# Kernel optimization log

Measured on AMD Instinct MI355X. Metric: run time of the kernel, lower is better.

## Reference

```python
import jax, jax.numpy as jnp
import numpy as np

H_WINDOW = 8
X_WINDOW = 8
H_LAG = 0
X_LAG = 0
CHANNELS = 1
B, T = 8192, 2048


def setup_inputs() -> dict:
    key = jax.random.key(0)
    k1, k2, k3 = jax.random.split(key, 3)
    h = jax.random.normal(k1, (B, T, 1), dtype=jnp.float32)
    # torch init: normal(0, 0.05)
    h_weights = 0.05 * jax.random.normal(k2, (H_WINDOW, CHANNELS), dtype=jnp.float32)
    x_weights = 0.05 * jax.random.normal(k3, (X_WINDOW, CHANNELS), dtype=jnp.float32)
    biases = jnp.zeros((1, CHANNELS), dtype=jnp.float32)
    return {"h": h, "h_weights": h_weights, "x_weights": x_weights, "biases": biases}


def reference(h, h_weights, x_weights, biases):
    b, t, _ = h.shape
    start_ix = max(H_WINDOW + H_LAG - 1, X_WINDOW, X_LAG - 1)
    h_t = jnp.transpose(h, (1, 0, 2))              # [T, B, 1] time-major for per-step gather
    hw0 = h[:, :H_WINDOW].reshape(b, H_WINDOW)     # initial h window
    xw0 = jnp.zeros((b, X_WINDOW), dtype=h.dtype)  # initial x window (zeros, as in torch)

    def step(carry, i):
        hw_, xw_ = carry  # [B, H_WINDOW], [B, X_WINDOW]
        out = xw_ @ x_weights + hw_ @ h_weights + biases  # [B, CHANNELS]
        # window updates; at the final step the torch code skips the update but the
        # carry is discarded, so an index-clamped unconditional update is equivalent
        idx = jnp.minimum(i + 1 - H_LAG, t - 1)
        hw_n = jnp.concatenate([hw_, h_t[idx]], axis=1)[:, -H_WINDOW:]
        xw_n = jnp.concatenate([xw_, out], axis=1)[:, -X_WINDOW:]
        return (hw_n, xw_n), out

    _, outs = jax.lax.scan(step, (hw0, xw0), jnp.arange(start_ix, t))  # [T-start_ix, B, C]
    output = jnp.zeros((b, t, CHANNELS), dtype=h.dtype)
    output = output.at[:, start_ix:].set(jnp.transpose(outs, (1, 0, 2)))
    return output
```

## Files before the change

### kernel.cpp

```cpp
#include <hip/hip_runtime.h>


typedef float  f32x4  __attribute__((ext_vector_type(4)));
typedef short  bf16x8 __attribute__((ext_vector_type(8)));

#define TT 2048
#define BB 8192
#define LK 64
#define NTAPS 71

__device__ __forceinline__ unsigned short f2bfu(float x) {
    unsigned u = __float_as_uint(x);
    return (unsigned short)((u + 0x7FFFu + ((u >> 16) & 1u)) >> 16);
}
__device__ __forceinline__ float bf2f(short s) {
    return __uint_as_float(((unsigned)(unsigned short)s) << 16);
}

__device__ __forceinline__ void group8(const float hwt[8], const float xwt[8],
                                       float bs, const float win[8],
                                       const float nh[8], const float xq[8],
                                       float res[8])
{
#pragma unroll
    for (int u = 0; u < 8; ++u) {
        float acc = bs;
#pragma unroll
        for (int k = u; k < 8; ++k) acc = fmaf(win[k], hwt[k - u], acc);
#pragma unroll
        for (int k = 0; k < u; ++k) acc = fmaf(nh[k], hwt[8 - u + k], acc);
#pragma unroll
        for (int k = u; k < 8; ++k) acc = fmaf(xq[k], xwt[k - u], acc);
#pragma unroll
        for (int k = 0; k < u; ++k) acc = fmaf(res[k], xwt[8 - u + k], acc);
        res[u] = acc;
    }
}

__global__ void rr_setup(const float* __restrict__ hwt_g, const float* __restrict__ xwt_g,
                         const float* __restrict__ bias_g, float* __restrict__ ws)
{
    if (threadIdx.x != 0 || blockIdx.x != 0) return;
    float hwt[8], xwt[8];
#pragma unroll
    for (int j = 0; j < 8; ++j) { hwt[j] = hwt_g[j]; xwt[j] = xwt_g[j]; }
    float K[LK];
    K[0] = 1.f;
    float ksum = 1.f;
#pragma unroll
    for (int n = 1; n < LK; ++n) {
        float a = 0.f;
#pragma unroll
        for (int j = 0; j < 8; ++j) {
            const int idx = n - 8 + j;
            if (idx >= 0) a = fmaf(xwt[j], K[idx], a);
        }
        K[n] = a; ksum += a;
    }
#pragma unroll
    for (int d = 0; d < NTAPS; ++d) {
        float a = 0.f;
#pragma unroll
        for (int j = 0; j < 8; ++j) {
            const int n = d - 7 + j;
            if (n >= 0 && n < LK) a = fmaf(hwt[j], K[n], a);
        }
        ws[d] = a;
    }
    ws[NTAPS] = bias_g[0] * ksum;
}

__global__ __launch_bounds__(256) void rr_mfma(
    const float* __restrict__ h, const float* __restrict__ hwt_g,
    const float* __restrict__ xwt_g, const float* __restrict__ bias_g,
    const float* __restrict__ cws, float* __restrict__ out)
{
    __shared__ short hlds[16][584];
    __shared__ float cl[72];

    const int t   = threadIdx.x;
    const int bid = blockIdx.x;
    const int strip = bid & 3;
    const int r0    = (bid >> 2) << 4;

    const int ts     = (strip < 3) ? (5 + 31 * strip) : 98;
    const int ntiles = (strip < 3) ? 31 : 30;
    const int gcol0  = 16 * ts - 80;
    const int nf4    = (strip < 3) ? 144 : 140;

    if (t < 72) cl[t] = cws[t];

    {
        const int row = t >> 4, l16 = t & 15;
        const float* hrow = h + (size_t)(r0 + row) * TT + gcol0;
#pragma unroll
        for (int k = 0; k < 9; ++k) {
            const int c = l16 + 16 * k;
            if (c < nf4) {
                float4 v = reinterpret_cast<const float4*>(hrow)[c];
                uint2 pk;
                pk.x = (unsigned)f2bfu(v.x) | ((unsigned)f2bfu(v.y) << 16);
                pk.y = (unsigned)f2bfu(v.z) | ((unsigned)f2bfu(v.w) << 16);
                *reinterpret_cast<uint2*>(&hlds[row][4 * c]) = pk;
            }
        }
    }
    __syncthreads();

    const int lane = t & 63;
    const int v    = lane & 15;
    const int gq   = lane >> 4;
    const int w    = t >> 6;

    const float biasK = cl[71];

    bf16x8 bfr[3];
#pragma unroll
    for (int kb = 0; kb < 3; ++kb) {
#pragma unroll
        for (int e = 0; e < 8; ++e) {
            const int idx = 80 + v - 32 * kb - 8 * gq - e;
            const float val = (idx >= 0 && idx < NTAPS) ? cl[idx] : 0.f;
            bfr[kb][e] = (short)f2bfu(val);
        }
    }

    for (int tl = w; tl < ntiles; tl += 4) {
        const int colb = 16 * tl;
        f32x4 acc = {0.f, 0.f, 0.f, 0.f};
#pragma unroll
        for (int kb = 0; kb < 3; ++kb) {
            const bf16x8 a = *reinterpret_cast<const bf16x8*>(
                &hlds[v][colb + 32 * kb + 8 * gq]);
            acc = __builtin_amdgcn_mfma_f32_16x16x32_bf16(a, bfr[kb], acc, 0, 0, 0);
        }
        const int i0 = (ts + tl) * 16;
        float* ob = out + (size_t)(r0 + 4 * gq) * TT + i0 + v;
#pragma unroll
        for (int q = 0; q < 4; ++q) ob[(size_t)q * TT] = acc[q] + biasK;
    }

    if (strip == 0 && t < 16) {
        const int row = t;
        float hwt[8], xwt[8];
#pragma unroll
        for (int j = 0; j < 8; ++j) { hwt[j] = hwt_g[j]; xwt[j] = xwt_g[j]; }
        const float bs = bias_g[0];
        float* orow = out + (size_t)(r0 + row) * TT;
        float win[8], xq[8];
#pragma unroll
        for (int j = 0; j < 8; ++j) { win[j] = bf2f(hlds[row][j]); xq[j] = 0.f; }
#pragma unroll
        for (int j = 0; j < 8; ++j) orow[j] = 0.f;
        for (int g = 8; g < 80; g += 8) {
            float nh[8], res[8];
#pragma unroll
            for (int j = 0; j < 8; ++j) nh[j] = bf2f(hlds[row][g + 1 + j]);
            group8(hwt, xwt, bs, win, nh, xq, res);
#pragma unroll
            for (int j = 0; j < 8; ++j) orow[g + j] = res[j];
#pragma unroll
            for (int j = 0; j < 8; ++j) { win[j] = nh[j]; xq[j] = res[j]; }
        }
    }
}

__global__ __launch_bounds__(64) void rr_fallback(
    const float* __restrict__ h, const float* __restrict__ hwt_g,
    const float* __restrict__ xwt_g, const float* __restrict__ bias_g,
    float* __restrict__ out)
{
    const int b = blockIdx.x * 64 + threadIdx.x;
    const float* __restrict__ hr = h + (size_t)b * TT;
    float* __restrict__ orow = out + (size_t)b * TT;
    float hwt[8], xwt[8];
#pragma unroll
    for (int j = 0; j < 8; ++j) { hwt[j] = hwt_g[j]; xwt[j] = xwt_g[j]; }
    const float bs = bias_g[0];
    float win[8], xq[8], nh[8];
#pragma unroll
    for (int j = 0; j < 8; ++j) { win[j] = hr[j]; xq[j] = 0.0f; }
#pragma unroll
    for (int j = 0; j < 8; ++j) nh[j] = hr[9 + j];
    float4 zz = make_float4(0.f, 0.f, 0.f, 0.f);
    *reinterpret_cast<float4*>(orow) = zz;
    *reinterpret_cast<float4*>(orow + 4) = zz;
    for (int g = 8; g < TT; g += 8) {
        float nn[8];
#pragma unroll
        for (int j = 0; j < 8; ++j) {
            int idx = g + 9 + j; if (idx > TT - 1) idx = TT - 1;
            nn[j] = hr[idx];
        }
        float res[8];
        group8(hwt, xwt, bs, win, nh, xq, res);
        *reinterpret_cast<float4*>(orow + g)     = make_float4(res[0], res[1], res[2], res[3]);
        *reinterpret_cast<float4*>(orow + g + 4) = make_float4(res[4], res[5], res[6], res[7]);
#pragma unroll
        for (int j = 0; j < 8; ++j) { win[j] = nh[j]; nh[j] = nn[j]; xq[j] = res[j]; }
    }
}

extern "C" void kernel_launch(void* const* d_in, const int* in_sizes, int n_in,
                              void* d_out, int out_size, void* d_ws, size_t ws_size,
                              hipStream_t stream) {
    const float* h    = (const float*)d_in[0];
    const float* hwt  = (const float*)d_in[1];
    const float* xwt  = (const float*)d_in[2];
    const float* bias = (const float*)d_in[3];
    float* out = (float*)d_out;

    if (ws_size >= (NTAPS + 1) * sizeof(float)) {
        float* ws = (float*)d_ws;
        rr_setup<<<1, 64, 0, stream>>>(hwt, xwt, bias, ws);
        rr_mfma<<<(BB / 16) * 4, 256, 0, stream>>>(h, hwt, xwt, bias, ws, out);
    } else {
        rr_fallback<<<BB / 64, 64, 0, stream>>>(h, hwt, xwt, bias, out);
    }
}
```

Measured before the change: 34.27 us.

## Fuse tap setup into main kernel and halve strips per row block

Removes the separate single-thread setup kernel by having thread 0 of every block compute the impulse-response taps into shared memory, overlapping with the h tile load. Each 16-row block now covers half the time axis instead of a quarter, cutting the redundant halo loads. The exact prefix recursion reads fp32 h from global memory instead of the bf16 LDS copy. In exchange, every block repeats the serial tap computation, LDS per block grows, and the grid has half as many blocks.

```diff
diff --git a/kernel.cpp b/kernel.cpp
--- a/kernel.cpp
+++ b/kernel.cpp
@@ -8,13 +8,11 @@
 #define BB 8192
 #define LK 64
 #define NTAPS 71
+#define LROW 1080
 
-__device__ __forceinline__ unsigned short f2bfu(float x) {
+__device__ __forceinline__ unsigned f2bfu(float x) {
     unsigned u = __float_as_uint(x);
-    return (unsigned short)((u + 0x7FFFu + ((u >> 16) & 1u)) >> 16);
-}
-__device__ __forceinline__ float bf2f(short s) {
-    return __uint_as_float(((unsigned)(unsigned short)s) << 16);
+    return (u + 0x7FFFu + ((u >> 16) & 1u)) >> 16;
 }
 
 __device__ __forceinline__ void group8(const float hwt[8], const float xwt[8],
@@ -37,89 +35,92 @@
     }
 }
 
-__global__ void rr_setup(const float* __restrict__ hwt_g, const float* __restrict__ xwt_g,
-                         const float* __restrict__ bias_g, float* __restrict__ ws)
-{
-    if (threadIdx.x != 0 || blockIdx.x != 0) return;
-    float hwt[8], xwt[8];
-#pragma unroll
-    for (int j = 0; j < 8; ++j) { hwt[j] = hwt_g[j]; xwt[j] = xwt_g[j]; }
-    float K[LK];
-    K[0] = 1.f;
-    float ksum = 1.f;
-#pragma unroll
-    for (int n = 1; n < LK; ++n) {
-        float a = 0.f;
-#pragma unroll
-        for (int j = 0; j < 8; ++j) {
-            const int idx = n - 8 + j;
-            if (idx >= 0) a = fmaf(xwt[j], K[idx], a);
-        }
-        K[n] = a; ksum += a;
-    }
-#pragma unroll
-    for (int d = 0; d < NTAPS; ++d) {
-        float a = 0.f;
-#pragma unroll
-        for (int j = 0; j < 8; ++j) {
-            const int n = d - 7 + j;
-            if (n >= 0 && n < LK) a = fmaf(hwt[j], K[n], a);
-        }
-        ws[d] = a;
-    }
-    ws[NTAPS] = bias_g[0] * ksum;
-}
-
-__global__ __launch_bounds__(256) void rr_mfma(
+__global__ __launch_bounds__(256) void rr_fused(
     const float* __restrict__ h, const float* __restrict__ hwt_g,
     const float* __restrict__ xwt_g, const float* __restrict__ bias_g,
-    const float* __restrict__ cws, float* __restrict__ out)
+    float* __restrict__ out)
 {
-    __shared__ short hlds[16][584];
-    __shared__ float cl[72];
+    __shared__ short hlds[16][LROW];
+    __shared__ float kl[LK];
+    __shared__ float cl[NTAPS + 1];
 
     const int t   = threadIdx.x;
     const int bid = blockIdx.x;
-    const int strip = bid & 3;
-    const int r0    = (bid >> 2) << 4;
+    const int s   = bid & 1;
+    const int r0  = (bid >> 1) << 4;
 
-    const int ts     = (strip < 3) ? (5 + 31 * strip) : 98;
-    const int ntiles = (strip < 3) ? 31 : 30;
-    const int gcol0  = 16 * ts - 80;
-    const int nf4    = (strip < 3) ? 144 : 140;
-
-    if (t < 72) cl[t] = cws[t];
+    const int ts     = s ? 67 : 5;
+    const int ntiles = s ? 61 : 62;
+    const int gcol0  = s ? 992 : 0;
+    const int nf4    = s ? 264 : 268;
 
     {
         const int row = t >> 4, l16 = t & 15;
         const float* hrow = h + (size_t)(r0 + row) * TT + gcol0;
 #pragma unroll
-        for (int k = 0; k < 9; ++k) {
+        for (int k = 0; k < 17; ++k) {
             const int c = l16 + 16 * k;
             if (c < nf4) {
                 float4 v = reinterpret_cast<const float4*>(hrow)[c];
                 uint2 pk;
-                pk.x = (unsigned)f2bfu(v.x) | ((unsigned)f2bfu(v.y) << 16);
-                pk.y = (unsigned)f2bfu(v.z) | ((unsigned)f2bfu(v.w) << 16);
+                pk.x = f2bfu(v.x) | (f2bfu(v.y) << 16);
+                pk.y = f2bfu(v.z) | (f2bfu(v.w) << 16);
                 *reinterpret_cast<uint2*>(&hlds[row][4 * c]) = pk;
             }
         }
     }
+
+    if (t == 0) {
+        float xw[8], hw[8];
+#pragma unroll
+        for (int j = 0; j < 8; ++j) { xw[j] = xwt_g[j]; hw[j] = hwt_g[j]; }
+        float w[8];
+#pragma unroll
+        for (int j = 0; j < 8; ++j) w[j] = 0.f;
+        float ksum = 0.f;
+        for (int n = 0; n < LK; ++n) {
+            float k;
+            if (n == 0) k = 1.f;
+            else {
+                k = 0.f;
+#pragma unroll
+                for (int j = 0; j < 8; ++j) k = fmaf(xw[j], w[j], k);
+            }
+            kl[n] = k; ksum += k;
+#pragma unroll
+            for (int j = 0; j < 7; ++j) w[j] = w[j + 1];
+            w[7] = k;
+        }
+        float v[8];
+#pragma unroll
+        for (int j = 0; j < 8; ++j) v[j] = 0.f;
+        for (int d = 0; d < NTAPS; ++d) {
+            const float nk = (d < LK) ? kl[d] : 0.f;
+#pragma unroll
+            for (int j = 0; j < 7; ++j) v[j] = v[j + 1];
+            v[7] = nk;
+            float ca = 0.f;
+#pragma unroll
+            for (int j = 0; j < 8; ++j) ca = fmaf(hw[j], v[j], ca);
+            cl[d] = ca;
+        }
+        cl[NTAPS] = bias_g[0] * ksum;
+    }
     __syncthreads();
 
     const int lane = t & 63;
-    const int v    = lane & 15;
+    const int v16  = lane & 15;
     const int gq   = lane >> 4;
     const int w    = t >> 6;
 
-    const float biasK = cl[71];
+    const float biasK = cl[NTAPS];
 
     bf16x8 bfr[3];
 #pragma unroll
     for (int kb = 0; kb < 3; ++kb) {
 #pragma unroll
         for (int e = 0; e < 8; ++e) {
-            const int idx = 80 + v - 32 * kb - 8 * gq - e;
+            const int idx = 80 + v16 - 32 * kb - 8 * gq - e;
             const float val = (idx >= 0 && idx < NTAPS) ? cl[idx] : 0.f;
             bfr[kb][e] = (short)f2bfu(val);
         }
@@ -131,73 +132,37 @@
 #pragma unroll
         for (int kb = 0; kb < 3; ++kb) {
             const bf16x8 a = *reinterpret_cast<const bf16x8*>(
-                &hlds[v][colb + 32 * kb + 8 * gq]);
+                &hlds[v16][colb + 32 * kb + 8 * gq]);
             acc = __builtin_amdgcn_mfma_f32_16x16x32_bf16(a, bfr[kb], acc, 0, 0, 0);
         }
         const int i0 = (ts + tl) * 16;
-        float* ob = out + (size_t)(r0 + 4 * gq) * TT + i0 + v;
+        float* ob = out + (size_t)(r0 + 4 * gq) * TT + i0 + v16;
 #pragma unroll
         for (int q = 0; q < 4; ++q) ob[(size_t)q * TT] = acc[q] + biasK;
     }
 
-    if (strip == 0 && t < 16) {
-        const int row = t;
+    if (s == 0 && t < 16) {
+        const float* hr = h + (size_t)(r0 + t) * TT;
+        float* orow = out + (size_t)(r0 + t) * TT;
         float hwt[8], xwt[8];
 #pragma unroll
         for (int j = 0; j < 8; ++j) { hwt[j] = hwt_g[j]; xwt[j] = xwt_g[j]; }
         const float bs = bias_g[0];
-        float* orow = out + (size_t)(r0 + row) * TT;
         float win[8], xq[8];
 #pragma unroll
-        for (int j = 0; j < 8; ++j) { win[j] = bf2f(hlds[row][j]); xq[j] = 0.f; }
+        for (int j = 0; j < 8; ++j) { win[j] = hr[j]; xq[j] = 0.f; }
 #pragma unroll
         for (int j = 0; j < 8; ++j) orow[j] = 0.f;
         for (int g = 8; g < 80; g += 8) {
             float nh[8], res[8];
 #pragma unroll
-            for (int j = 0; j < 8; ++j) nh[j] = bf2f(hlds[row][g + 1 + j]);
+            for (int j = 0; j < 8; ++j) nh[j] = hr[g + 1 + j];
             group8(hwt, xwt, bs, win, nh, xq, res);
 #pragma unroll
             for (int j = 0; j < 8; ++j) orow[g + j] = res[j];
 #pragma unroll
             for (int j = 0; j < 8; ++j) { win[j] = nh[j]; xq[j] = res[j]; }
         }
-    }
-}
-
-__global__ __launch_bounds__(64) void rr_fallback(
-    const float* __restrict__ h, const float* __restrict__ hwt_g,
-    const float* __restrict__ xwt_g, const float* __restrict__ bias_g,
-    float* __restrict__ out)
-{
-    const int b = blockIdx.x * 64 + threadIdx.x;
-    const float* __restrict__ hr = h + (size_t)b * TT;
-    float* __restrict__ orow = out + (size_t)b * TT;
-    float hwt[8], xwt[8];
-#pragma unroll
-    for (int j = 0; j < 8; ++j) { hwt[j] = hwt_g[j]; xwt[j] = xwt_g[j]; }
-    const float bs = bias_g[0];
-    float win[8], xq[8], nh[8];
-#pragma unroll
-    for (int j = 0; j < 8; ++j) { win[j] = hr[j]; xq[j] = 0.0f; }
-#pragma unroll
-    for (int j = 0; j < 8; ++j) nh[j] = hr[9 + j];
-    float4 zz = make_float4(0.f, 0.f, 0.f, 0.f);
-    *reinterpret_cast<float4*>(orow) = zz;
-    *reinterpret_cast<float4*>(orow + 4) = zz;
-    for (int g = 8; g < TT; g += 8) {
-        float nn[8];
-#pragma unroll
-        for (int j = 0; j < 8; ++j) {
-            int idx = g + 9 + j; if (idx > TT - 1) idx = TT - 1;
-            nn[j] = hr[idx];
-        }
-        float res[8];
-        group8(hwt, xwt, bs, win, nh, xq, res);
-        *reinterpret_cast<float4*>(orow + g)     = make_float4(res[0], res[1], res[2], res[3]);
-        *reinterpret_cast<float4*>(orow + g + 4) = make_float4(res[4], res[5], res[6], res[7]);
-#pragma unroll
-        for (int j = 0; j < 8; ++j) { win[j] = nh[j]; nh[j] = nn[j]; xq[j] = res[j]; }
     }
 }
 
@@ -209,12 +174,5 @@
     const float* xwt  = (const float*)d_in[2];
     const float* bias = (const float*)d_in[3];
     float* out = (float*)d_out;
-
-    if (ws_size >= (NTAPS + 1) * sizeof(float)) {
-        float* ws = (float*)d_ws;
-        rr_setup<<<1, 64, 0, stream>>>(hwt, xwt, bias, ws);
-        rr_mfma<<<(BB / 16) * 4, 256, 0, stream>>>(h, hwt, xwt, bias, ws, out);
-    } else {
-        rr_fallback<<<BB / 64, 64, 0, stream>>>(h, hwt, xwt, bias, out);
-    }
+    rr_fused<<<(BB / 16) * 2, 256, 0, stream>>>(h, hwt, xwt, bias, out);
 }
```

Measured after the change: 35.98 us. +5.0%, slower.
